# Kernel optimization log

Measured on AMD Instinct MI355X. Metric: run time of the kernel, lower is better.

Reference implementation:

```python
import jax, jax.numpy as jnp
import numpy as np

N_QUBITS = 10
QLCU_LAYERS = 2
GATE_LAYERS = 2
FEATURE_DIM = 256
OUTPUT_DIM = 1
BATCH = 2048
TWO_PI = float(2.0 * np.pi)
N_MEAS = 3 * N_QUBITS


def _ang(theta, B):
    # broadcast scalar or (B,) angle to (B,) float32
    return jnp.broadcast_to(jnp.asarray(theta, jnp.float32), (B,))


def _apply_1q(psi, U, wire):
    # psi: (B,)+(2,)*n ; U: (B,2,2) complex64
    pm = jnp.moveaxis(psi, wire + 1, -1)
    out = jnp.einsum('bij,b...j->b...i', U, pm)
    return jnp.moveaxis(out, -1, wire + 1)


def rx(psi, theta, wire):
    B = psi.shape[0]
    t = _ang(theta, B) * 0.5
    c = jnp.cos(t).astype(jnp.complex64)
    s = (-1j) * jnp.sin(t).astype(jnp.complex64)
    U = jnp.stack([jnp.stack([c, s], -1), jnp.stack([s, c], -1)], -2)
    return _apply_1q(psi, U, wire)


def ry(psi, theta, wire):
    B = psi.shape[0]
    t = _ang(theta, B) * 0.5
    c = jnp.cos(t).astype(jnp.complex64)
    s = jnp.sin(t).astype(jnp.complex64)
    U = jnp.stack([jnp.stack([c, -s], -1), jnp.stack([s, c], -1)], -2)
    return _apply_1q(psi, U, wire)


def rz(psi, theta, wire):
    # diagonal: e^{-i t/2}, e^{+i t/2}
    B = psi.shape[0]
    n = psi.ndim - 1
    t = _ang(theta, B) * 0.5
    ph = jnp.exp(1j * jnp.stack([-t, t], -1).astype(jnp.complex64))  # (B,2)
    pm = jnp.moveaxis(psi, wire + 1, -1)
    pm = pm * ph.reshape((B,) + (1,) * (n - 1) + (2,))
    return jnp.moveaxis(pm, -1, wire + 1)


def _mv2(psi, a, b):
    return jnp.moveaxis(psi, (a + 1, b + 1), (-2, -1))


def _mv2_back(pm, a, b):
    return jnp.moveaxis(pm, (-2, -1), (a + 1, b + 1))


def crz(psi, theta, control, target):
    # diagonal on (control,target): [1, 1, e^{-it/2}, e^{+it/2}]
    B = psi.shape[0]
    n = psi.ndim - 1
    t = (_ang(theta, B) * 0.5).astype(jnp.complex64)
    e_m = jnp.exp(-1j * t)
    e_p = jnp.exp(1j * t)
    one = jnp.ones_like(e_m)
    P = jnp.stack([jnp.stack([one, one], -1), jnp.stack([e_m, e_p], -1)], -2)  # (B,2,2)
    pm = _mv2(psi, control, target)
    pm = pm * P.reshape((B,) + (1,) * (n - 2) + (2, 2))
    return _mv2_back(pm, control, target)


def ising_xx(psi, theta, a, b):
    # exp(-i t/2 XX): cos(t/2) I - i sin(t/2) X(x)X (bit-flip both)
    B = psi.shape[0]
    n = psi.ndim - 1
    t = _ang(theta, B) * 0.5
    c = jnp.cos(t).astype(jnp.complex64).reshape((B,) + (1,) * n)
    s = jnp.sin(t).astype(jnp.complex64).reshape((B,) + (1,) * n)
    pm = _mv2(psi, a, b)
    out = c * pm - 1j * s * pm[..., ::-1, ::-1]
    return _mv2_back(out, a, b)


def ising_yy(psi, theta, a, b):
    # exp(-i t/2 YY): (YY psi)[ta,tb] = (-1 if ta==tb else +1) * psi[flip]
    B = psi.shape[0]
    n = psi.ndim - 1
    t = _ang(theta, B) * 0.5
    c = jnp.cos(t).astype(jnp.complex64).reshape((B,) + (1,) * n)
    s = jnp.sin(t).astype(jnp.complex64).reshape((B,) + (1,) * n)
    sign = jnp.array([[-1.0, 1.0], [1.0, -1.0]], jnp.complex64)
    pm = _mv2(psi, a, b)
    out = c * pm - 1j * s * sign * pm[..., ::-1, ::-1]
    return _mv2_back(out, a, b)


def measure_xyz(psi):
    # expvals [X0..X_{n-1}, Y0.., Z0..] -> (B, 3n) float32
    n = psi.ndim - 1
    xs, ys, zs = [], [], []
    for w in range(n):
        pm = jnp.moveaxis(psi, w + 1, -1)
        p0, p1 = pm[..., 0], pm[..., 1]
        axes = tuple(range(1, n))
        a = jnp.sum(jnp.conj(p0) * p1, axis=axes)
        xs.append(2.0 * jnp.real(a))
        ys.append(2.0 * jnp.imag(a))
        zs.append(jnp.sum(jnp.abs(p0) ** 2 - jnp.abs(p1) ** 2, axis=axes))
    return jnp.stack(xs + ys + zs, axis=1).astype(jnp.float32)


def selective_ssm(psi, qlcu, bpar, cpar, dtpar, n, layers):
    idx = 0
    for _ in range(layers):
        for i in range(n):
            psi = ry(psi, qlcu[:, idx], i); idx += 1
        for i in range(n):
            psi = ising_xx(psi, qlcu[:, idx], i, (i + 1) % n); idx += 1
        for i in range(n):
            psi = ry(psi, bpar[i], i)
        for i in range(n):
            psi = ry(psi, qlcu[:, idx], i); idx += 1
        for i in range(n):
            psi = ising_yy(psi, qlcu[:, idx], i, (i + 1) % n); idx += 1
        for i in range(n):
            psi = rz(psi, cpar[i], i)
        for i in range(n):
            psi = rx(psi, dtpar[i], i)
    return psi


def gating(psi, gp, n, layers):
    idx = 0
    for _ in range(layers):
        for i in range(n):
            psi = rx(psi, gp[idx], i); idx += 1
        for i in range(n - 1):
            psi = crz(psi, gp[idx], i, i + 1); idx += 1
        for i in range(n):
            psi = ry(psi, gp[idx], i); idx += 1
        if n > 1:
            psi = crz(psi, gp[idx], n - 1, 0); idx += 1
    return psi


def skip_circuit(psi, sp, n):
    idx = 0
    for i in range(n):
        psi = rx(psi, sp[idx], i); idx += 1
    for i in range(n):
        psi = ry(psi, sp[idx], i); idx += 1
    for i in range(n):
        psi = rz(psi, sp[idx], i); idx += 1
    return psi


def _forward(x, W_proj, b_proj, qlcu_base, gate_base, skip_base, b_params, c_params, dt_params,
             W1, b1, W2, b2, W3, b3, w1, w2, w3, W_out, b_out):
    B = x.shape[0]
    n = N_QUBITS
    proj = x @ W_proj.T + b_proj
    qlcu = jax.nn.sigmoid(proj) * TWO_PI + qlcu_base[None, :]
    psi0 = jnp.zeros((B, 2 ** n), jnp.complex64).at[:, 0].set(1.0).reshape((B,) + (2,) * n)
    m1 = measure_xyz(selective_ssm(psi0, qlcu, b_params, c_params, dt_params, n, QLCU_LAYERS))
    # branches 2/3 have batch-independent params and initial state -> compute once, broadcast
    psi1 = jnp.zeros((1, 2 ** n), jnp.complex64).at[:, 0].set(1.0).reshape((1,) + (2,) * n)
    m2 = jnp.broadcast_to(measure_xyz(gating(psi1, gate_base, n, GATE_LAYERS)), (B, N_MEAS))
    m3 = jnp.broadcast_to(measure_xyz(skip_circuit(psi1, skip_base, n)), (B, N_MEAS))
    y1 = m1 @ W1.T + b1
    y2 = m2 @ W2.T + b2
    y3 = m3 @ W3.T + b3
    comb = w1 * y1 + w2 * y2 + w3 * y3
    return comb @ W_out.T + b_out


def setup_inputs() -> dict:
    key = jax.random.key(0)
    ks = jax.random.split(key, 17)
    nq = N_QUBITS
    n_qlcu = 4 * nq * QLCU_LAYERS
    n_gate = 4 * nq * GATE_LAYERS
    n_skip = 3 * nq
    lim_p = 1.0 / np.sqrt(FEATURE_DIM)
    lim_m = 1.0 / np.sqrt(N_MEAS)
    return dict(
        x=jax.random.normal(ks[0], (BATCH, FEATURE_DIM), jnp.float32),
        W_proj=jax.random.uniform(ks[1], (n_qlcu, FEATURE_DIM), jnp.float32, -lim_p, lim_p),
        b_proj=jax.random.uniform(ks[2], (n_qlcu,), jnp.float32, -lim_p, lim_p),
        qlcu_base=jax.random.uniform(ks[3], (n_qlcu,), jnp.float32, 0.0, TWO_PI),
        gate_base=jax.random.uniform(ks[4], (n_gate,), jnp.float32, 0.0, TWO_PI),
        skip_base=jax.random.uniform(ks[5], (n_skip,), jnp.float32, 0.0, TWO_PI),
        b_params=jax.random.uniform(ks[6], (nq,), jnp.float32, 0.0, TWO_PI),
        c_params=jax.random.uniform(ks[7], (nq,), jnp.float32, 0.0, TWO_PI),
        dt_params=jax.random.uniform(ks[8], (nq,), jnp.float32, 0.0, TWO_PI),
        W1=jax.random.uniform(ks[9], (N_MEAS, N_MEAS), jnp.float32, -lim_m, lim_m),
        b1=jax.random.uniform(ks[10], (N_MEAS,), jnp.float32, -lim_m, lim_m),
        W2=jax.random.uniform(ks[11], (N_MEAS, N_MEAS), jnp.float32, -lim_m, lim_m),
        b2=jax.random.uniform(ks[12], (N_MEAS,), jnp.float32, -lim_m, lim_m),
        W3=jax.random.uniform(ks[13], (N_MEAS, N_MEAS), jnp.float32, -lim_m, lim_m),
        b3=jax.random.uniform(ks[14], (N_MEAS,), jnp.float32, -lim_m, lim_m),
        w1=jnp.ones((1,), jnp.float32),
        w2=jnp.ones((1,), jnp.float32),
        w3=jnp.ones((1,), jnp.float32),
        W_out=jax.random.uniform(ks[15], (OUTPUT_DIM, N_MEAS), jnp.float32, -lim_m, lim_m),
        b_out=jax.random.uniform(ks[16], (OUTPUT_DIM,), jnp.float32, -lim_m, lim_m),
    )


def reference(x, W_proj, b_proj, qlcu_base, gate_base, skip_base, b_params, c_params, dt_params,
              W1, b1, W2, b2, W3, b3, w1, w2, w3, W_out, b_out):
    return _forward(x, W_proj, b_proj, qlcu_base, gate_base, skip_base, b_params, c_params, dt_params,
                    W1, b1, W2, b2, W3, b3, w1, w2, w3, W_out, b_out)
```

## Files before the change

### kernel.cpp

```cpp
#include <hip/hip_runtime.h>
#include <math.h>

#define TPB 320
#define TWO_PI_F 6.283185307179586f


#define ALLQ(OP) OP(0) OP(1) OP(2) OP(3) OP(4) OP(5) OP(6) OP(7) OP(8) OP(9)
#define ALLQ9(OP) OP(0) OP(1) OP(2) OP(3) OP(4) OP(5) OP(6) OP(7) OP(8)

template<int CTRL>
__device__ __forceinline__ float dppmv(float v) {
    return __builtin_bit_cast(float,
        __builtin_amdgcn_update_dpp(0, __builtin_bit_cast(int, v), CTRL, 0xF, 0xF, true));
}

template<int LM>
__device__ __forceinline__ float lx(float v, int lane) {
    (void)lane;
    if constexpr (LM == 1)       return dppmv<0xB1>(v);
    else if constexpr (LM == 2)  return dppmv<0x4E>(v);
    else if constexpr (LM == 3)  return dppmv<0x1B>(v);
    else if constexpr (LM == 4)  return dppmv<0x1B>(dppmv<0x141>(v));
    else if constexpr (LM == 6)  return dppmv<0xB1>(dppmv<0x141>(v));
    else if constexpr (LM == 8)  return dppmv<0x128>(v);
    else if constexpr (LM == 12) return dppmv<0x1B>(dppmv<0x140>(v));
    else                         return __shfl_xor(v, LM);
}


template<int W>
__device__ __forceinline__ void g_ry(float (&re)[16], float (&im)[16], float c, float s, int lane) {
    if constexpr (W <= 5) {
        constexpr int LM = 1 << (5 - W);
        const float ss = ((lane >> (5 - W)) & 1) ? s : -s;
        float pr[16], pi[16];
#pragma unroll
        for (int r = 0; r < 16; ++r) { pr[r] = lx<LM>(re[r], lane); pi[r] = lx<LM>(im[r], lane); }
#pragma unroll
        for (int r = 0; r < 16; ++r) {
            re[r] = fmaf(ss, pr[r], c * re[r]);
            im[r] = fmaf(ss, pi[r], c * im[r]);
        }
    } else {
        constexpr int MK = 1 << (9 - W);
#pragma unroll
        for (int r = 0; r < 16; ++r) {
            if ((r & MK) == 0) {
                const int r1 = r | MK;
                float r0 = re[r], i0 = im[r], r1v = re[r1], i1 = im[r1];
                re[r]  = fmaf(-s, r1v, c * r0);
                im[r]  = fmaf(-s, i1,  c * i0);
                re[r1] = fmaf( s, r0,  c * r1v);
                im[r1] = fmaf( s, i0,  c * i1);
            }
        }
    }
}

template<int W>
__device__ __forceinline__ void g_rx(float (&re)[16], float (&im)[16], float c, float s, int lane) {
    if constexpr (W <= 5) {
        constexpr int LM = 1 << (5 - W);
        float pr[16], pi[16];
#pragma unroll
        for (int r = 0; r < 16; ++r) { pr[r] = lx<LM>(re[r], lane); pi[r] = lx<LM>(im[r], lane); }
#pragma unroll
        for (int r = 0; r < 16; ++r) {
            re[r] = fmaf( s, pi[r], c * re[r]);
            im[r] = fmaf(-s, pr[r], c * im[r]);
        }
    } else {
        constexpr int MK = 1 << (9 - W);
#pragma unroll
        for (int r = 0; r < 16; ++r) {
            if ((r & MK) == 0) {
                const int r1 = r | MK;
                float r0 = re[r], i0 = im[r], r1v = re[r1], i1 = im[r1];
                re[r]  = fmaf( s, i1,  c * r0);
                im[r]  = fmaf(-s, r1v, c * i0);
                re[r1] = fmaf( s, i0,  c * r1v);
                im[r1] = fmaf(-s, r0,  c * i1);
            }
        }
    }
}

template<int W>
__device__ __forceinline__ void g_rz(float (&re)[16], float (&im)[16], float c, float s, int lane) {
    if constexpr (W <= 5) {
        const float sp = ((lane >> (5 - W)) & 1) ? s : -s;
#pragma unroll
        for (int r = 0; r < 16; ++r) {
            float rr = re[r], ii = im[r];
            re[r] = rr * c - ii * sp;
            im[r] = ii * c + rr * sp;
        }
    } else {
        constexpr int MK = 1 << (9 - W);
#pragma unroll
        for (int r = 0; r < 16; ++r) {
            const float sp = (r & MK) ? s : -s;
            float rr = re[r], ii = im[r];
            re[r] = rr * c - ii * sp;
            im[r] = ii * c + rr * sp;
        }
    }
}

template<int C, int T>
__device__ __forceinline__ void g_crz(float (&re)[16], float (&im)[16], float c, float s, int lane) {
#pragma unroll
    for (int r = 0; r < 16; ++r) {
        const int cb = (C <= 5) ? ((lane >> (5 - C)) & 1) : ((r >> (9 - C)) & 1);
        const int tb = (T <= 5) ? ((lane >> (5 - T)) & 1) : ((r >> (9 - T)) & 1);
        const float cc  = cb ? c : 1.f;
        const float sp2 = cb ? (tb ? s : -s) : 0.f;
        float rr = re[r], ii = im[r];
        re[r] = cc * rr - sp2 * ii;
        im[r] = cc * ii + sp2 * rr;
    }
}

template<int A, int Bq, bool YY>
__device__ __forceinline__ void g_xy(float (&re)[16], float (&im)[16], float c, float s, int lane) {
    constexpr int bpA = 9 - A, bpB = 9 - Bq;
    constexpr int LM   = ((bpA >= 4) ? (1 << (bpA - 4)) : 0) | ((bpB >= 4) ? (1 << (bpB - 4)) : 0);
    constexpr int LOCM = ((bpA < 4) ? (1 << bpA) : 0) | ((bpB < 4) ? (1 << bpB) : 0);
    float pr[16], pi[16];
#pragma unroll
    for (int r = 0; r < 16; ++r) {
        float vr = re[r ^ LOCM], vi = im[r ^ LOCM];
        if constexpr (LM != 0) { pr[r] = lx<LM>(vr, lane); pi[r] = lx<LM>(vi, lane); }
        else                   { pr[r] = vr; pi[r] = vi; }
    }
#pragma unroll
    for (int r = 0; r < 16; ++r) {
        float sg;
        if constexpr (YY) {
            const int bA = (A  <= 5) ? ((lane >> (5 - A )) & 1) : ((r >> (9 - A )) & 1);
            const int bB = (Bq <= 5) ? ((lane >> (5 - Bq)) & 1) : ((r >> (9 - Bq)) & 1);
            sg = (bA == bB) ? -s : s;
        } else sg = s;
        float rr = re[r], ii = im[r];
        re[r] = fmaf( sg, pi[r], c * rr);
        im[r] = fmaf(-sg, pr[r], c * ii);
    }
}

template<int W>
__device__ __forceinline__ void g_u1(float (&re)[16], float (&im)[16], const float* U, int lane) {
    const float u00r=U[0], u00i=U[1], u01r=U[2], u01i=U[3];
    const float u10r=U[4], u10i=U[5], u11r=U[6], u11i=U[7];
    if constexpr (W <= 5) {
        constexpr int LM = 1 << (5 - W);
        const int side = (lane >> (5 - W)) & 1;
        const float aR = side ? u11r : u00r, aI = side ? u11i : u00i;
        const float bR = side ? u10r : u01r, bI = side ? u10i : u01i;
        float pr[16], pi[16];
#pragma unroll
        for (int r = 0; r < 16; ++r) { pr[r] = lx<LM>(re[r], lane); pi[r] = lx<LM>(im[r], lane); }
#pragma unroll
        for (int r = 0; r < 16; ++r) {
            float rr = re[r], ii = im[r];
            float nr = aR * rr; nr = fmaf(-aI, ii, nr); nr = fmaf(bR, pr[r], nr); nr = fmaf(-bI, pi[r], nr);
            float ni = aR * ii; ni = fmaf( aI, rr, ni); ni = fmaf(bR, pi[r], ni); ni = fmaf( bI, pr[r], ni);
            re[r] = nr; im[r] = ni;
        }
    } else {
        constexpr int MK = 1 << (9 - W);
#pragma unroll
        for (int r = 0; r < 16; ++r) {
            if ((r & MK) == 0) {
                const int r1 = r | MK;
                float r0 = re[r], i0 = im[r], r1v = re[r1], i1 = im[r1];
                float a = u00r*r0; a = fmaf(-u00i, i0, a); a = fmaf(u01r, r1v, a); a = fmaf(-u01i, i1, a);
                float b = u00r*i0; b = fmaf( u00i, r0, b); b = fmaf(u01r, i1,  b); b = fmaf( u01i, r1v, b);
                float c = u10r*r0; c = fmaf(-u10i, i0, c); c = fmaf(u11r, r1v, c); c = fmaf(-u11i, i1, c);
                float d = u10r*i0; d = fmaf( u10i, r0, d); d = fmaf(u11r, i1,  d); d = fmaf( u11i, r1v, d);
                re[r] = a; im[r] = b; re[r1] = c; im[r1] = d;
            }
        }
    }
}

__device__ __forceinline__ float wred(float v, int lane) {
    v += lx<1>(v, lane); v += lx<2>(v, lane); v += lx<4>(v, lane);
    v += lx<8>(v, lane); v += lx<16>(v, lane); v += lx<32>(v, lane);
    return v;
}

template<int W>
__device__ __forceinline__ void meas_q(const float (&re)[16], const float (&im)[16], int lane,
                                       float& X, float& Y, float& Z) {
    float xa = 0.f, ya = 0.f, za = 0.f;
    if constexpr (W <= 5) {
        constexpr int LM = 1 << (5 - W);
        const float sg = ((lane >> (5 - W)) & 1) ? -1.f : 1.f;
        float pr[16], pi[16];
#pragma unroll
        for (int r = 0; r < 16; ++r) { pr[r] = lx<LM>(re[r], lane); pi[r] = lx<LM>(im[r], lane); }
#pragma unroll
        for (int r = 0; r < 16; ++r) {
            xa = fmaf(re[r], pr[r], xa); xa = fmaf(im[r], pi[r], xa);
            ya = fmaf(re[r], pi[r], ya); ya = fmaf(-im[r], pr[r], ya);
            za = fmaf(re[r], re[r], za); za = fmaf(im[r], im[r], za);
        }
        ya *= sg; za *= sg;
    } else {
        constexpr int MK = 1 << (9 - W);
#pragma unroll
        for (int r = 0; r < 16; ++r) {
            if ((r & MK) == 0) {
                const int r1 = r | MK;
                xa += 2.f * (re[r] * re[r1] + im[r] * im[r1]);
                ya += 2.f * (re[r] * im[r1] - im[r] * re[r1]);
                za += (re[r] * re[r] + im[r] * im[r]) - (re[r1] * re[r1] + im[r1] * im[r1]);
            }
        }
    }
    X = wred(xa, lane); Y = wred(ya, lane); Z = wred(za, lane);
}

__device__ __forceinline__ void init_state(float (&re)[16], float (&im)[16], int lane) {
#pragma unroll
    for (int r = 0; r < 16; ++r) { re[r] = 0.f; im[r] = 0.f; }
    if (lane == 0) re[0] = 1.f;
}


__device__ void branch_gating(const float* __restrict__ gb,
                              const float* __restrict__ b1,
                              const float* __restrict__ W2, const float* __restrict__ b2,
                              const float* __restrict__ w1p, const float* __restrict__ w2p,
                              const float* __restrict__ Wout, const float* __restrict__ bout,
                              float* __restrict__ ws_c, int lane) {
    float re[16], im[16];
    const bool act = lane < 30;
    const int kk = act ? lane : 0;
    float y2 = 0.f;

    init_state(re, im, lane);
    for (int L = 0; L < 2; ++L) {
        const int g0 = L * 30;
#define G_RX(i) { float s_, c_; __sincosf(0.5f * gb[g0 + i], &s_, &c_); g_rx<i>(re, im, c_, s_, lane); }
        ALLQ(G_RX)
#undef G_RX
#define G_CRZ(i) { float s_, c_; __sincosf(0.5f * gb[g0 + 10 + i], &s_, &c_); g_crz<i, i + 1>(re, im, c_, s_, lane); }
        ALLQ9(G_CRZ)
#undef G_CRZ
#define G_RY(i) { float s_, c_; __sincosf(0.5f * gb[g0 + 19 + i], &s_, &c_); g_ry<i>(re, im, c_, s_, lane); }
        ALLQ(G_RY)
#undef G_RY
        { float s_, c_; __sincosf(0.5f * gb[g0 + 29], &s_, &c_); g_crz<9, 0>(re, im, c_, s_, lane); }
    }
#define G_M2(w) { float X, Y, Z; meas_q<w>(re, im, lane, X, Y, Z); \
        y2 = fmaf(X, W2[kk * 30 + w], y2); y2 = fmaf(Y, W2[kk * 30 + 10 + w], y2); y2 = fmaf(Z, W2[kk * 30 + 20 + w], y2); }
    ALLQ(G_M2)
#undef G_M2

    const float w1v = w1p[0], w2v = w2p[0];
    float vk = act ? Wout[kk] * (w1v * b1[kk] + w2v * (b2[kk] + y2)) : 0.f;
    vk = wred(vk, lane);
    if (lane == 0) ws_c[0] = vk + bout[0];
}

__device__ void branch_skip(const float* __restrict__ sp,
                            const float* __restrict__ W3, const float* __restrict__ b3,
                            const float* __restrict__ w3p,
                            const float* __restrict__ Wout,
                            float* __restrict__ ws_c, int lane) {
    float re[16], im[16];
    const bool act = lane < 30;
    const int kk = act ? lane : 0;
    float y3 = 0.f;

    init_state(re, im, lane);
#define G_RXS(i) { float s_, c_; __sincosf(0.5f * sp[i], &s_, &c_); g_rx<i>(re, im, c_, s_, lane); }
    ALLQ(G_RXS)
#undef G_RXS
#define G_RYS(i) { float s_, c_; __sincosf(0.5f * sp[10 + i], &s_, &c_); g_ry<i>(re, im, c_, s_, lane); }
    ALLQ(G_RYS)
#undef G_RYS
#define G_RZS(i) { float s_, c_; __sincosf(0.5f * sp[20 + i], &s_, &c_); g_rz<i>(re, im, c_, s_, lane); }
    ALLQ(G_RZS)
#undef G_RZS
#define G_M3(w) { float X, Y, Z; meas_q<w>(re, im, lane, X, Y, Z); \
        y3 = fmaf(X, W3[kk * 30 + w], y3); y3 = fmaf(Y, W3[kk * 30 + 10 + w], y3); y3 = fmaf(Z, W3[kk * 30 + 20 + w], y3); }
    ALLQ(G_M3)
#undef G_M3

    const float w3v = w3p[0];
    float vk = act ? Wout[kk] * (w3v * (b3[kk] + y3)) : 0.f;
    vk = wred(vk, lane);
    if (lane == 0) ws_c[0] = vk;
}


__global__ void __launch_bounds__(TPB) k_main(
    const float* __restrict__ x, const float* __restrict__ Wp,
    const float* __restrict__ bp_, const float* __restrict__ qb,
    const float* __restrict__ bpar, const float* __restrict__ cpar, const float* __restrict__ dtpar,
    const float* __restrict__ gb, const float* __restrict__ sp,
    const float* __restrict__ W1, const float* __restrict__ b1,
    const float* __restrict__ W2, const float* __restrict__ b2,
    const float* __restrict__ W3, const float* __restrict__ b3,
    const float* __restrict__ w1p, const float* __restrict__ w2p, const float* __restrict__ w3p,
    const float* __restrict__ Wout, const float* __restrict__ bout,
    float* __restrict__ ws, int B) {

    const int wv = threadIdx.x >> 6, lane = threadIdx.x & 63;

    if (wv == 4) {
        if (blockIdx.x == 0) {
            branch_gating(gb, b1, W2, b2, w1p, w2p, Wout, bout, ws + B, lane);
            if (gridDim.x == 1) branch_skip(sp, W3, b3, w3p, Wout, ws + B + 1, lane);
        } else if (blockIdx.x == 1) {
            branch_skip(sp, W3, b3, w3p, Wout, ws + B + 1, lane);
        }
        return;
    }

    const int b = blockIdx.x * 4 + wv;
    const int bb = (b < B) ? b : (B - 1);

    __shared__ float proj[4][80];
    __shared__ float ac1[4][10], as1[4][10], ac2[4][10], as2[4][10];
    __shared__ float gc[4][60], gs[4][60];
    __shared__ float ub[4][80];
    __shared__ float uraw[4][32], uu[4][32];

    const int sub = lane & 15, grp = lane >> 4;
    float4 xv[4];
    {
        const float* xr = x + (size_t)bb * 256 + sub * 16;
#pragma unroll
        for (int j = 0; j < 4; ++j) xv[j] = reinterpret_cast<const float4*>(xr)[j];
    }
#pragma unroll 4
    for (int p = 0; p < 20; ++p) {
        const int row = p * 4 + grp;
        const float* wr = Wp + (size_t)row * 256 + sub * 16;
        float acc = 0.f;
#pragma unroll
        for (int j = 0; j < 4; ++j) {
            float4 w4 = reinterpret_cast<const float4*>(wr)[j];
            acc = fmaf(xv[j].x, w4.x, acc); acc = fmaf(xv[j].y, w4.y, acc);
            acc = fmaf(xv[j].z, w4.z, acc); acc = fmaf(xv[j].w, w4.w, acc);
        }
        acc += lx<1>(acc, lane); acc += lx<2>(acc, lane);
        acc += lx<4>(acc, lane); acc += lx<8>(acc, lane);
        if (sub == 0) proj[wv][row] = acc;
    }

    {
#define DO_ANGLE(IDX) { \
        const int idx = (IDX); \
        float ang = TWO_PI_F / (1.f + __expf(-(proj[wv][idx] + bp_[idx]))) + qb[idx]; \
        const int l = (idx >= 40) ? 1 : 0; \
        const int p = idx - 40 * l; \
        float s_, c_; \
        if (p < 10) { \
            __sincosf(0.5f * ang, &s_, &c_); \
            if (l == 0) { ac1[wv][p] = c_; as1[wv][p] = s_; } \
            else        { ac2[wv][p] = c_; as2[wv][p] = s_; } \
        } else if (p < 20) { \
            __sincosf(0.5f * ang, &s_, &c_); \
            gc[wv][l * 30 + p - 10] = c_; gs[wv][l * 30 + p - 10] = s_; \
        } else if (p < 30) { \
            __sincosf(0.5f * (ang + bpar[p - 20]), &s_, &c_); \
            gc[wv][l * 30 + 10 + p - 20] = c_; gs[wv][l * 30 + 10 + p - 20] = s_; \
        } else { \
            __sincosf(0.5f * ang, &s_, &c_); \
            gc[wv][l * 30 + 20 + p - 30] = c_; gs[wv][l * 30 + 20 + p - 30] = s_; \
        } }
        DO_ANGLE(lane)
        if (lane < 16) DO_ANGLE(64 + lane)
#undef DO_ANGLE

        if (lane < 30) {
            float ut = 0.f;
            for (int k = 0; k < 30; ++k) ut = fmaf(Wout[k], W1[k * 30 + lane], ut);
            uraw[wv][lane] = w1p[0] * ut;
        }
        if (lane < 10) {
            float ca = ac2[wv][lane], sa = as2[wv][lane];
            float cg2, sg2, cd2, sd2;
            __sincosf(0.5f * cpar[lane],  &sg2, &cg2);
            __sincosf(0.5f * dtpar[lane], &sd2, &cd2);
            float A = ca * cd2, Bv = sa * sd2;
            float C = -sa * cd2, D = -ca * sd2;
            float E = sa * cd2,  F = -ca * sd2;
            float G = ca * cd2,  H = -sa * sd2;
            float* U = &ub[wv][lane * 8];
            U[0] = cg2 * A + sg2 * Bv;  U[1] = cg2 * Bv - sg2 * A;
            U[2] = cg2 * C - sg2 * D;   U[3] = sg2 * C + cg2 * D;
            U[4] = cg2 * E + sg2 * F;   U[5] = cg2 * F - sg2 * E;
            U[6] = cg2 * G - sg2 * H;   U[7] = sg2 * G + cg2 * H;

            float cg, sgf, cd, sdf;
            __sincosf(cpar[lane],  &sgf, &cg);
            __sincosf(dtpar[lane], &sdf, &cd);
            float uX = uraw[wv][lane], uY = uraw[wv][10 + lane], uZ = uraw[wv][20 + lane];
            uu[wv][lane]      =  uX * cg + uY * cd * sgf + uZ * sdf * sgf;
            uu[wv][10 + lane] = -uX * sgf + uY * cd * cg + uZ * sdf * cg;
            uu[wv][20 + lane] = -uY * sdf + uZ * cd;
        }
    }

    float re[16], im[16];
    {
        const float* AC = ac1[wv]; const float* AS = as1[wv];
        float pl = ((lane >> 5) & 1) ? AS[0] : AC[0];
        pl *= ((lane >> 4) & 1) ? AS[1] : AC[1];
        pl *= ((lane >> 3) & 1) ? AS[2] : AC[2];
        pl *= ((lane >> 2) & 1) ? AS[3] : AC[3];
        pl *= ((lane >> 1) & 1) ? AS[4] : AC[4];
        pl *= ( lane       & 1) ? AS[5] : AC[5];
#pragma unroll
        for (int r = 0; r < 16; ++r) {
            float p = ((r >> 3) & 1) ? AS[6] : AC[6];
            p *= ((r >> 2) & 1) ? AS[7] : AC[7];
            p *= ((r >> 1) & 1) ? AS[8] : AC[8];
            p *= ( r       & 1) ? AS[9] : AC[9];
            re[r] = pl * p; im[r] = 0.f;
        }
    }

    const float* GC = gc[wv]; const float* GS = gs[wv];
#define G_XX1(i) g_xy<i, (i + 1) % 10, false>(re, im, GC[i], GS[i], lane);
    ALLQ(G_XX1)
#undef G_XX1
#define G_CD1(i) g_ry<i>(re, im, GC[10 + i], GS[10 + i], lane);
    ALLQ(G_CD1)
#undef G_CD1
#define G_YY1(i) g_xy<i, (i + 1) % 10, true>(re, im, GC[20 + i], GS[20 + i], lane);
    ALLQ(G_YY1)
#undef G_YY1
#define G_UB(i) g_u1<i>(re, im, &ub[wv][i * 8], lane);
    ALLQ(G_UB)
#undef G_UB
#define G_XX2(i) g_xy<i, (i + 1) % 10, false>(re, im, GC[30 + i], GS[30 + i], lane);
    ALLQ(G_XX2)
#undef G_XX2
#define G_CD2(i) g_ry<i>(re, im, GC[40 + i], GS[40 + i], lane);
    ALLQ(G_CD2)
#undef G_CD2
#define G_YY2(i) g_xy<i, (i + 1) % 10, true>(re, im, GC[50 + i], GS[50 + i], lane);
    ALLQ(G_YY2)
#undef G_YY2

    float n2[16], n2s = 0.f;
#pragma unroll
    for (int r = 0; r < 16; ++r) { n2[r] = fmaf(re[r], re[r], im[r] * im[r]); n2s += n2[r]; }

    const float* U = uu[wv];
    float oacc = 0.f;

#define M_LANE(w, LM_) { \
        float pr[16], pi[16]; \
        _Pragma("unroll") \
        for (int r = 0; r < 16; ++r) { pr[r] = lx<LM_>(re[r], lane); pi[r] = lx<LM_>(im[r], lane); } \
        float xa = 0.f, ya = 0.f; \
        _Pragma("unroll") \
        for (int r = 0; r < 16; ++r) { \
            xa = fmaf(re[r], pr[r], xa); xa = fmaf(im[r], pi[r], xa); \
            ya = fmaf(re[r], pi[r], ya); ya = fmaf(-im[r], pr[r], ya); \
        } \
        const float sg = ((lane >> (5 - w)) & 1) ? -1.f : 1.f; \
        oacc = fmaf(xa, U[w], oacc); \
        oacc = fmaf(sg * ya, U[10 + w], oacc); \
        oacc = fmaf(sg * n2s, U[20 + w], oacc); }
    M_LANE(0, 32) M_LANE(1, 16) M_LANE(2, 8) M_LANE(3, 4) M_LANE(4, 2) M_LANE(5, 1)
#undef M_LANE

#define M_REG(w, MK) { \
        float xa = 0.f, ya = 0.f, za = 0.f; \
        _Pragma("unroll") \
        for (int r = 0; r < 16; ++r) { \
            if ((r & MK) == 0) { \
                const int r1 = r | MK; \
                xa = fmaf(re[r], re[r1], xa); xa = fmaf(im[r], im[r1], xa); \
                ya = fmaf(re[r], im[r1], ya); ya = fmaf(-im[r], re[r1], ya); \
                za += n2[r] - n2[r1]; \
            } } \
        oacc = fmaf(2.f * xa, U[w], oacc); \
        oacc = fmaf(2.f * ya, U[10 + w], oacc); \
        oacc = fmaf(za, U[20 + w], oacc); }
    M_REG(6, 8) M_REG(7, 4) M_REG(8, 2) M_REG(9, 1)
#undef M_REG

    oacc = wred(oacc, lane);
    if (lane == 0 && b < B) ws[b] = oacc;
}

__global__ void k_out(const float* __restrict__ ws, float* __restrict__ out, int B) {
    int i = blockIdx.x * blockDim.x + threadIdx.x;
    if (i < B) out[i] = ws[i] + ws[B] + ws[B + 1];
}

extern "C" void kernel_launch(void* const* d_in, const int* in_sizes, int n_in,
                              void* d_out, int out_size, void* d_ws, size_t ws_size,
                              hipStream_t stream) {
    const float* x         = (const float*)d_in[0];
    const float* W_proj    = (const float*)d_in[1];
    const float* b_proj    = (const float*)d_in[2];
    const float* qlcu_base = (const float*)d_in[3];
    const float* gate_base = (const float*)d_in[4];
    const float* skip_base = (const float*)d_in[5];
    const float* b_params  = (const float*)d_in[6];
    const float* c_params  = (const float*)d_in[7];
    const float* dt_params = (const float*)d_in[8];
    const float* W1    = (const float*)d_in[9];
    const float* b1    = (const float*)d_in[10];
    const float* W2    = (const float*)d_in[11];
    const float* b2    = (const float*)d_in[12];
    const float* W3    = (const float*)d_in[13];
    const float* b3    = (const float*)d_in[14];
    const float* w1    = (const float*)d_in[15];
    const float* w2    = (const float*)d_in[16];
    const float* w3    = (const float*)d_in[17];
    const float* W_out = (const float*)d_in[18];
    const float* b_out = (const float*)d_in[19];
    float* out = (float*)d_out;
    float* ws  = (float*)d_ws;

    const int B = in_sizes[0] / 256;
    const int nb = (B + 3) / 4;

    hipLaunchKernelGGL(k_main, dim3(nb), dim3(TPB), 0, stream,
                       x, W_proj, b_proj, qlcu_base, b_params, c_params, dt_params,
                       gate_base, skip_base, W1, b1, W2, b2, W3, b3, w1, w2, w3,
                       W_out, b_out, ws, B);
    hipLaunchKernelGGL(k_out, dim3((B + 255) / 256), dim3(256), 0, stream, ws, out, B);
}
```

Before: 56.16 us.

## Fuse lane-crossing gate pairs on qubits 0/1 and reorder ring gates

Single-qubit gates on the two wires held across lanes 32/16 are merged into one two-qubit tensor-product update. The first and last ring XX/YY gates, which touch wires 1/2 and 9/0, are combined into one update, and the ring is reordered to start at wire 1. Measurements for qubits 0 and 1 now use neighbour values fetched right after the last gate. The aim is to cut the number of cross-lane permutes and dependent passes over the 32 register amplitudes. The cost is more live registers, since six 16-element buffers are held at once, which could lower occupancy or cause spills.

```diff
diff --git a/kernel.cpp b/kernel.cpp
--- a/kernel.cpp
+++ b/kernel.cpp
@@ -180,6 +180,98 @@
                 re[r] = a; im[r] = b; re[r1] = c; im[r1] = d;
             }
         }
+    }
+}
+
+
+__device__ __forceinline__ void g_ry2_01(float (&re)[16], float (&im)[16],
+                                         float c0, float s0, float c1, float s1, int lane) {
+    float ar[16], ai[16], br[16], bi[16], cr2[16], ci2[16];
+#pragma unroll
+    for (int r = 0; r < 16; ++r) { ar[r] = lx<32>(re[r], lane); ai[r] = lx<32>(im[r], lane); }
+#pragma unroll
+    for (int r = 0; r < 16; ++r) { br[r] = lx<16>(re[r], lane); bi[r] = lx<16>(im[r], lane); }
+#pragma unroll
+    for (int r = 0; r < 16; ++r) { cr2[r] = lx<48>(re[r], lane); ci2[r] = lx<48>(im[r], lane); }
+    const float sg0 = ((lane >> 5) & 1) ? s0 : -s0;
+    const float sg1 = ((lane >> 4) & 1) ? s1 : -s1;
+    const float k0 = c0 * c1, k1 = c1 * sg0, k2 = c0 * sg1, k3 = sg0 * sg1;
+#pragma unroll
+    for (int r = 0; r < 16; ++r) {
+        float o_r = k0 * re[r];
+        o_r = fmaf(k1, ar[r], o_r); o_r = fmaf(k2, br[r], o_r); o_r = fmaf(k3, cr2[r], o_r);
+        float o_i = k0 * im[r];
+        o_i = fmaf(k1, ai[r], o_i); o_i = fmaf(k2, bi[r], o_i); o_i = fmaf(k3, ci2[r], o_i);
+        re[r] = o_r; im[r] = o_i;
+    }
+}
+
+__device__ __forceinline__ void g_u2_01(float (&re)[16], float (&im)[16],
+                                        const float* U0, const float* U1, int lane) {
+    const int b0 = (lane >> 5) & 1, b1 = (lane >> 4) & 1;
+    const float u0o_r = U0[(b0*2+b0)*2],       u0o_i = U0[(b0*2+b0)*2+1];
+    const float u0f_r = U0[(b0*2+(b0^1))*2],   u0f_i = U0[(b0*2+(b0^1))*2+1];
+    const float u1o_r = U1[(b1*2+b1)*2],       u1o_i = U1[(b1*2+b1)*2+1];
+    const float u1f_r = U1[(b1*2+(b1^1))*2],   u1f_i = U1[(b1*2+(b1^1))*2+1];
+    const float K00r = u0o_r*u1o_r - u0o_i*u1o_i, K00i = u0o_r*u1o_i + u0o_i*u1o_r;
+    const float K01r = u0o_r*u1f_r - u0o_i*u1f_i, K01i = u0o_r*u1f_i + u0o_i*u1f_r;
+    const float K10r = u0f_r*u1o_r - u0f_i*u1o_i, K10i = u0f_r*u1o_i + u0f_i*u1o_r;
+    const float K11r = u0f_r*u1f_r - u0f_i*u1f_i, K11i = u0f_r*u1f_i + u0f_i*u1f_r;
+    float ar[16], ai[16], br[16], bi[16], cr2[16], ci2[16];
+#pragma unroll
+    for (int r = 0; r < 16; ++r) { ar[r] = lx<32>(re[r], lane); ai[r] = lx<32>(im[r], lane); }
+#pragma unroll
+    for (int r = 0; r < 16; ++r) { br[r] = lx<16>(re[r], lane); bi[r] = lx<16>(im[r], lane); }
+#pragma unroll
+    for (int r = 0; r < 16; ++r) { cr2[r] = lx<48>(re[r], lane); ci2[r] = lx<48>(im[r], lane); }
+#pragma unroll
+    for (int r = 0; r < 16; ++r) {
+        float rr = re[r], ii = im[r];
+        float o_r = K00r * rr;         o_r = fmaf(-K00i, ii, o_r);
+        o_r = fmaf(K01r, br[r], o_r);  o_r = fmaf(-K01i, bi[r], o_r);
+        o_r = fmaf(K10r, ar[r], o_r);  o_r = fmaf(-K10i, ai[r], o_r);
+        o_r = fmaf(K11r, cr2[r], o_r); o_r = fmaf(-K11i, ci2[r], o_r);
+        float o_i = K00r * ii;         o_i = fmaf(K00i, rr, o_i);
+        o_i = fmaf(K01r, bi[r], o_i);  o_i = fmaf(K01i, br[r], o_i);
+        o_i = fmaf(K10r, ai[r], o_i);  o_i = fmaf(K10i, ar[r], o_i);
+        o_i = fmaf(K11r, ci2[r], o_i); o_i = fmaf(K11i, cr2[r], o_i);
+        re[r] = o_r; im[r] = o_i;
+    }
+}
+
+__device__ __forceinline__ void g_ring2(float (&re)[16], float (&im)[16],
+                                        float ca, float sa, float cb, float sb,
+                                        bool yy, int lane) {
+    float ar[16], ai[16], br[16], bi[16], cr2[16], ci2[16];
+#pragma unroll
+    for (int r = 0; r < 16; ++r) { ar[r] = lx<24>(re[r], lane); ai[r] = lx<24>(im[r], lane); }
+#pragma unroll
+    for (int r = 0; r < 16; ++r) { br[r] = lx<32>(re[r ^ 1], lane); bi[r] = lx<32>(im[r ^ 1], lane); }
+#pragma unroll
+    for (int r = 0; r < 16; ++r) { cr2[r] = lx<56>(re[r ^ 1], lane); ci2[r] = lx<56>(im[r ^ 1], lane); }
+    float ka, kb0, kb1, kab0, kab1;
+    if (yy) {
+        const bool ea = (((lane >> 4) & 1) == ((lane >> 3) & 1));
+        const float sga = ea ? -sa : sa;
+        const int b0l = (lane >> 5) & 1;
+        const float sgb0 = (0 == b0l) ? -sb : sb;
+        const float sgb1 = (1 == b0l) ? -sb : sb;
+        ka = cb * sga; kb0 = ca * sgb0; kb1 = ca * sgb1;
+        kab0 = sga * sgb0; kab1 = sga * sgb1;
+    } else {
+        ka = cb * sa; kb0 = kb1 = ca * sb; kab0 = kab1 = sa * sb;
+    }
+    const float k0 = ca * cb;
+#pragma unroll
+    for (int r = 0; r < 16; ++r) {
+        const float kb  = (r & 1) ? kb1  : kb0;
+        const float kab = (r & 1) ? kab1 : kab0;
+        float rr = re[r], ii = im[r];
+        float o_r = k0 * rr;
+        o_r = fmaf(ka, ai[r], o_r); o_r = fmaf(kb, bi[r], o_r); o_r = fmaf(-kab, cr2[r], o_r);
+        float o_i = k0 * ii;
+        o_i = fmaf(-ka, ar[r], o_i); o_i = fmaf(-kb, br[r], o_i); o_i = fmaf(-kab, ci2[r], o_i);
+        re[r] = o_r; im[r] = o_i;
     }
 }
 
@@ -427,34 +519,48 @@
     }
 
     const float* GC = gc[wv]; const float* GS = gs[wv];
-#define G_XX1(i) g_xy<i, (i + 1) % 10, false>(re, im, GC[i], GS[i], lane);
-    ALLQ(G_XX1)
-#undef G_XX1
+
+#define RING(base, YYf) \
+    g_ring2(re, im, GC[(base)+1], GS[(base)+1], GC[(base)+9], GS[(base)+9], YYf, lane); \
+    g_xy<2, 3, YYf>(re, im, GC[(base)+2], GS[(base)+2], lane); \
+    g_xy<3, 4, YYf>(re, im, GC[(base)+3], GS[(base)+3], lane); \
+    g_xy<4, 5, YYf>(re, im, GC[(base)+4], GS[(base)+4], lane); \
+    g_xy<5, 6, YYf>(re, im, GC[(base)+5], GS[(base)+5], lane); \
+    g_xy<6, 7, YYf>(re, im, GC[(base)+6], GS[(base)+6], lane); \
+    g_xy<7, 8, YYf>(re, im, GC[(base)+7], GS[(base)+7], lane); \
+    g_xy<8, 9, YYf>(re, im, GC[(base)+8], GS[(base)+8], lane); \
+    g_xy<0, 1, YYf>(re, im, GC[(base)+0], GS[(base)+0], lane);
+
+    RING(0, false)
+    g_ry2_01(re, im, GC[10], GS[10], GC[11], GS[11], lane);
 #define G_CD1(i) g_ry<i>(re, im, GC[10 + i], GS[10 + i], lane);
-    ALLQ(G_CD1)
+    G_CD1(2) G_CD1(3) G_CD1(4) G_CD1(5) G_CD1(6) G_CD1(7) G_CD1(8) G_CD1(9)
 #undef G_CD1
-#define G_YY1(i) g_xy<i, (i + 1) % 10, true>(re, im, GC[20 + i], GS[20 + i], lane);
-    ALLQ(G_YY1)
-#undef G_YY1
+    RING(20, true)
+    g_u2_01(re, im, &ub[wv][0], &ub[wv][8], lane);
 #define G_UB(i) g_u1<i>(re, im, &ub[wv][i * 8], lane);
-    ALLQ(G_UB)
+    G_UB(2) G_UB(3) G_UB(4) G_UB(5) G_UB(6) G_UB(7) G_UB(8) G_UB(9)
 #undef G_UB
-#define G_XX2(i) g_xy<i, (i + 1) % 10, false>(re, im, GC[30 + i], GS[30 + i], lane);
-    ALLQ(G_XX2)
-#undef G_XX2
+    RING(30, false)
+    g_ry2_01(re, im, GC[40], GS[40], GC[41], GS[41], lane);
 #define G_CD2(i) g_ry<i>(re, im, GC[40 + i], GS[40 + i], lane);
-    ALLQ(G_CD2)
+    G_CD2(2) G_CD2(3) G_CD2(4) G_CD2(5) G_CD2(6) G_CD2(7) G_CD2(8) G_CD2(9)
 #undef G_CD2
-#define G_YY2(i) g_xy<i, (i + 1) % 10, true>(re, im, GC[50 + i], GS[50 + i], lane);
-    ALLQ(G_YY2)
-#undef G_YY2
-
-    float n2[16], n2s = 0.f;
-#pragma unroll
-    for (int r = 0; r < 16; ++r) { n2[r] = fmaf(re[r], re[r], im[r] * im[r]); n2s += n2[r]; }
+    RING(50, true)
+#undef RING
 
     const float* U = uu[wv];
     float oacc = 0.f;
+
+    float q0r[16], q0i[16], q1r[16], q1i[16];
+#pragma unroll
+    for (int r = 0; r < 16; ++r) { q0r[r] = lx<32>(re[r], lane); q0i[r] = lx<32>(im[r], lane); }
+#pragma unroll
+    for (int r = 0; r < 16; ++r) { q1r[r] = lx<16>(re[r], lane); q1i[r] = lx<16>(im[r], lane); }
+
+    float n2[16], n2s = 0.f;
+#pragma unroll
+    for (int r = 0; r < 16; ++r) { n2[r] = fmaf(re[r], re[r], im[r] * im[r]); n2s += n2[r]; }
 
 #define M_LANE(w, LM_) { \
         float pr[16], pi[16]; \
@@ -470,7 +576,7 @@
         oacc = fmaf(xa, U[w], oacc); \
         oacc = fmaf(sg * ya, U[10 + w], oacc); \
         oacc = fmaf(sg * n2s, U[20 + w], oacc); }
-    M_LANE(0, 32) M_LANE(1, 16) M_LANE(2, 8) M_LANE(3, 4) M_LANE(4, 2) M_LANE(5, 1)
+    M_LANE(2, 8) M_LANE(3, 4) M_LANE(4, 2) M_LANE(5, 1)
 #undef M_LANE
 
 #define M_REG(w, MK) { \
@@ -488,6 +594,31 @@
         oacc = fmaf(za, U[20 + w], oacc); }
     M_REG(6, 8) M_REG(7, 4) M_REG(8, 2) M_REG(9, 1)
 #undef M_REG
+
+    {
+        float xa = 0.f, ya = 0.f;
+#pragma unroll
+        for (int r = 0; r < 16; ++r) {
+            xa = fmaf(re[r], q0r[r], xa); xa = fmaf(im[r], q0i[r], xa);
+            ya = fmaf(re[r], q0i[r], ya); ya = fmaf(-im[r], q0r[r], ya);
+        }
+        const float sg = ((lane >> 5) & 1) ? -1.f : 1.f;
+        oacc = fmaf(xa, U[0], oacc);
+        oacc = fmaf(sg * ya, U[10], oacc);
+        oacc = fmaf(sg * n2s, U[20], oacc);
+    }
+    {
+        float xa = 0.f, ya = 0.f;
+#pragma unroll
+        for (int r = 0; r < 16; ++r) {
+            xa = fmaf(re[r], q1r[r], xa); xa = fmaf(im[r], q1i[r], xa);
+            ya = fmaf(re[r], q1i[r], ya); ya = fmaf(-im[r], q1r[r], ya);
+        }
+        const float sg = ((lane >> 4) & 1) ? -1.f : 1.f;
+        oacc = fmaf(xa, U[1], oacc);
+        oacc = fmaf(sg * ya, U[11], oacc);
+        oacc = fmaf(sg * n2s, U[21], oacc);
+    }
 
     oacc = wred(oacc, lane);
     if (lane == 0 && b < B) ws[b] = oacc;
```

Result: no change. 55.87 us (-0.5%).
